# Optimization experiments

Hardware: AMD Instinct MI355X
Metric: run time of the kernel (lower is better)

## Reference

```python
import jax, jax.numpy as jnp
import numpy as np

N = 8192
D_IN, D_GAT, D_GCN = 128, 64, 64


def setup_inputs() -> dict:
    key = jax.random.key(0)
    ks = jax.random.split(key, 7)
    feat = jax.random.normal(ks[0], (N, D_IN), dtype=jnp.float32)
    r = jax.random.uniform(ks[1], (N, N), dtype=jnp.float32)
    sup = jnp.where(r < 0.01, r * 100.0, 0.0)
    xav = lambda k, shape: jax.random.normal(k, shape, dtype=jnp.float32) * jnp.sqrt(2.0 / (shape[0] + shape[1]))
    W_map = xav(ks[2], (D_IN, D_GAT))
    b_map = jnp.zeros((1,), dtype=jnp.float32)
    U = xav(ks[3], (D_GAT, 1))
    V = xav(ks[4], (D_GAT, 1))
    W_gcn = xav(ks[5], (D_GAT, D_GCN))
    return {"feat": feat, "sup": sup, "W_map": W_map, "b_map": b_map, "U": U, "V": V, "W_gcn": W_gcn}


def reference(feat, sup, W_map, b_map, U, V, W_gcn):
    n = sup.shape[0]
    sup2 = sup + jnp.eye(n, dtype=sup.dtype)  # add self-loops
    # GAT layer
    h = feat @ W_map                            # [N, D_GAT]
    s = h @ U                                   # [N, 1] score from source node i
    t = h @ V                                   # [N, 1] score from target node j
    # torch loop builds att[j, i] = tanh(s_i + t_j + b)
    att = jnp.tanh(s.T + t + b_map)             # [N, N]
    att = jnp.where(sup2 > 0, att, jnp.float32(-100.0))
    att = jax.nn.softmax(att, axis=1)
    gat_feat = jnp.tanh(att @ h)                # [N, D_GAT]
    # GCN layer (dropout is identity at inference)
    agg = sup2 @ gat_feat                       # [N, D_GAT]
    out = jax.nn.relu(agg @ W_gcn)              # [N, D_GCN]
    norm = jnp.linalg.norm(out, axis=1, keepdims=True)
    out = out / jnp.maximum(norm, jnp.float32(1e-12))  # F.normalize(p=2, dim=1)
    return out
```

## Files before the change

### kernel.cpp

```cpp
#include <hip/hip_runtime.h>


#define N_NODES 8192
#define D_IN    128
#define D_GAT   64
#define SLOTS   256

#define COMPACT4(VX, QQ)                                                      \
    {                                                                         \
        float ee[4] = {VX.x, VX.y, VX.z, VX.w};                               \
        _Pragma("unroll")                                                     \
        for (int u = 0; u < 4; ++u) {                                         \
            const int i = (QQ) * 4 + u;                                       \
            const float vv = ee[u] + ((i == j) ? 1.0f : 0.0f);      \
            const bool keep = vv > 0.f;                                       \
            const unsigned long long mask = __ballot(keep);                   \
            if (keep) {                                                       \
                const int pos = base +                                        \
                    __popcll(mask & ((1ull << lane) - 1ull));                 \
                if (pos < SLOTS) { clr[pos] = i; vvr[pos] = vv; }             \
            }                                                                 \
            base += __popcll(mask);                                           \
        }                                                                     \
    }

__global__ __launch_bounds__(256) void k1_map(
    const float* __restrict__ feat, const float* __restrict__ W_map,
    const float* __restrict__ U, const float* __restrict__ V,
    float* __restrict__ h, float* __restrict__ s, float* __restrict__ t)
{
    const int wid  = threadIdx.x >> 6;
    const int lane = threadIdx.x & 63;
    const int row = blockIdx.x * 4 + wid;
    __shared__ float f[4 * D_IN];
    if (threadIdx.x < 128)
        ((float4*)f)[threadIdx.x] =
            ((const float4*)(feat + (size_t)blockIdx.x * 4 * D_IN))[threadIdx.x];
    __syncthreads();
    const float* fr = f + wid * D_IN;
    float acc = 0.f;
#pragma unroll 8
    for (int k = 0; k < D_IN; ++k)
        acc += fr[k] * W_map[k * D_GAT + lane];
    h[row * D_GAT + lane] = acc;
    float sv = acc * U[lane];
    float tv = acc * V[lane];
#pragma unroll
    for (int off = 32; off > 0; off >>= 1) {
        sv += __shfl_xor(sv, off);
        tv += __shfl_xor(tv, off);
    }
    if (lane == 0) { s[row] = sv; t[row] = tv; }
}

__global__ __launch_bounds__(256) void k23_compact_gat(
    const float* __restrict__ sup, const float* __restrict__ h,
    const float* __restrict__ s, const float* __restrict__ t,
    const float* __restrict__ b,
    int* __restrict__ cnt, int* __restrict__ col, float* __restrict__ val,
    float* __restrict__ gat)
{
    const int wid  = threadIdx.x >> 6;
    const int lane = threadIdx.x & 63;
    const int j = blockIdx.x * 4 + wid;

    __shared__ int   cl_s[4][SLOTS];
    __shared__ float vv_s[4][SLOTS];
    __shared__ float w_s[4][SLOTS];
    int*   clr = cl_s[wid];
    float* vvr = vv_s[wid];
    float* w   = w_s[wid];

    const float4* row4 = (const float4*)(sup + (size_t)j * N_NODES);
    int base = 0;
    for (int q = lane; q < N_NODES / 4; q += 128) {
        float4 v0 = row4[q];
        float4 v1 = row4[q + 64];
        COMPACT4(v0, q);
        COMPACT4(v1, q + 64);
    }
    const int m = (base < SLOTS) ? base : SLOTS;
    __syncthreads();

    int*   colj = col + j * SLOTS;
    float* valj = val + j * SLOTS;
    const float tj = t[j] + b[0];
    float lmax = -1e30f;
    for (int p = lane; p < m; p += 64) {
        const int ci = clr[p];
        colj[p] = ci;
        valj[p] = vvr[p];
        const float e = tanhf(s[ci] + tj);
        w[p] = e;
        lmax = fmaxf(lmax, e);
    }
    if (lane == 0) cnt[j] = m;
#pragma unroll
    for (int off = 32; off > 0; off >>= 1)
        lmax = fmaxf(lmax, __shfl_xor(lmax, off));

    float lsum = 0.f;
    for (int p = lane; p < m; p += 64) {
        const float e = __expf(w[p] - lmax);
        w[p] = e;
        lsum += e;
    }
#pragma unroll
    for (int off = 32; off > 0; off >>= 1) lsum += __shfl_xor(lsum, off);
    __syncthreads();

    const int c16 = (lane & 15) * 4;
    const int pp  = lane >> 4;
    float4 a0 = make_float4(0,0,0,0), a1 = a0, a2 = a0, a3 = a0;
    for (int bse = 0; bse < m; bse += 16) {
        const int p0 = bse + pp, p1 = p0 + 4, p2 = p0 + 8, p3 = p0 + 12;
        if (p0 < m) { const float wp = w[p0];
            const float4 v = *(const float4*)(h + clr[p0] * D_GAT + c16);
            a0.x += wp*v.x; a0.y += wp*v.y; a0.z += wp*v.z; a0.w += wp*v.w; }
        if (p1 < m) { const float wp = w[p1];
            const float4 v = *(const float4*)(h + clr[p1] * D_GAT + c16);
            a1.x += wp*v.x; a1.y += wp*v.y; a1.z += wp*v.z; a1.w += wp*v.w; }
        if (p2 < m) { const float wp = w[p2];
            const float4 v = *(const float4*)(h + clr[p2] * D_GAT + c16);
            a2.x += wp*v.x; a2.y += wp*v.y; a2.z += wp*v.z; a2.w += wp*v.w; }
        if (p3 < m) { const float wp = w[p3];
            const float4 v = *(const float4*)(h + clr[p3] * D_GAT + c16);
            a3.x += wp*v.x; a3.y += wp*v.y; a3.z += wp*v.z; a3.w += wp*v.w; }
    }
    float4 acc;
    acc.x = (a0.x + a1.x) + (a2.x + a3.x);
    acc.y = (a0.y + a1.y) + (a2.y + a3.y);
    acc.z = (a0.z + a1.z) + (a2.z + a3.z);
    acc.w = (a0.w + a1.w) + (a2.w + a3.w);
#pragma unroll
    for (int off = 16; off <= 32; off <<= 1) {
        acc.x += __shfl_xor(acc.x, off); acc.y += __shfl_xor(acc.y, off);
        acc.z += __shfl_xor(acc.z, off); acc.w += __shfl_xor(acc.w, off);
    }
    if (pp == 0) {
        const float inv = 1.0f / lsum;
        float4 o;
        o.x = tanhf(acc.x * inv); o.y = tanhf(acc.y * inv);
        o.z = tanhf(acc.z * inv); o.w = tanhf(acc.w * inv);
        *(float4*)(gat + j * D_GAT + c16) = o;
    }
}

__global__ __launch_bounds__(256) void k4_gcn(
    const float* __restrict__ gat, const float* __restrict__ W_gcn,
    const int* __restrict__ cnt, const int* __restrict__ col,
    const float* __restrict__ val, float* __restrict__ out)
{
    const int wid  = threadIdx.x >> 6;
    const int lane = threadIdx.x & 63;
    const int j = blockIdx.x * 4 + wid;
    const int m = cnt[j];
    const int*   colj = col + j * SLOTS;
    const float* valj = val + j * SLOTS;
    __shared__ int   cl_s[4][SLOTS];
    __shared__ float wv_s[4][SLOTS];
    __shared__ float a_s[4][D_GAT];
    int*   cl = cl_s[wid];
    float* wv = wv_s[wid];
    float* a  = a_s[wid];
    for (int p = lane; p < m; p += 64) { cl[p] = colj[p]; wv[p] = valj[p]; }
    __syncthreads();

    const int c16 = (lane & 15) * 4;
    const int pp  = lane >> 4;
    float4 a0 = make_float4(0,0,0,0), a1 = a0, a2 = a0, a3 = a0;
    for (int base = 0; base < m; base += 16) {
        const int p0 = base + pp, p1 = p0 + 4, p2 = p0 + 8, p3 = p0 + 12;
        if (p0 < m) { const float wp = wv[p0];
            const float4 v = *(const float4*)(gat + cl[p0] * D_GAT + c16);
            a0.x += wp*v.x; a0.y += wp*v.y; a0.z += wp*v.z; a0.w += wp*v.w; }
        if (p1 < m) { const float wp = wv[p1];
            const float4 v = *(const float4*)(gat + cl[p1] * D_GAT + c16);
            a1.x += wp*v.x; a1.y += wp*v.y; a1.z += wp*v.z; a1.w += wp*v.w; }
        if (p2 < m) { const float wp = wv[p2];
            const float4 v = *(const float4*)(gat + cl[p2] * D_GAT + c16);
            a2.x += wp*v.x; a2.y += wp*v.y; a2.z += wp*v.z; a2.w += wp*v.w; }
        if (p3 < m) { const float wp = wv[p3];
            const float4 v = *(const float4*)(gat + cl[p3] * D_GAT + c16);
            a3.x += wp*v.x; a3.y += wp*v.y; a3.z += wp*v.z; a3.w += wp*v.w; }
    }
    float4 acc;
    acc.x = (a0.x + a1.x) + (a2.x + a3.x);
    acc.y = (a0.y + a1.y) + (a2.y + a3.y);
    acc.z = (a0.z + a1.z) + (a2.z + a3.z);
    acc.w = (a0.w + a1.w) + (a2.w + a3.w);
#pragma unroll
    for (int off = 16; off <= 32; off <<= 1) {
        acc.x += __shfl_xor(acc.x, off); acc.y += __shfl_xor(acc.y, off);
        acc.z += __shfl_xor(acc.z, off); acc.w += __shfl_xor(acc.w, off);
    }
    if (pp == 0) *(float4*)(a + c16) = acc;
    __syncthreads();

    float o = 0.f;
#pragma unroll 8
    for (int d = 0; d < D_GAT; ++d)
        o += a[d] * W_gcn[d * D_GAT + lane];
    o = fmaxf(o, 0.f);

    float ss = o * o;
#pragma unroll
    for (int off = 32; off > 0; off >>= 1) ss += __shfl_xor(ss, off);
    const float nrm = sqrtf(ss);
    out[j * D_GAT + lane] = o / fmaxf(nrm, 1e-12f);
}

extern "C" void kernel_launch(void* const* d_in, const int* in_sizes, int n_in,
                              void* d_out, int out_size, void* d_ws, size_t ws_size,
                              hipStream_t stream) {
    const float* feat  = (const float*)d_in[0];
    const float* sup   = (const float*)d_in[1];
    const float* W_map = (const float*)d_in[2];
    const float* b_map = (const float*)d_in[3];
    const float* U     = (const float*)d_in[4];
    const float* V     = (const float*)d_in[5];
    const float* W_gcn = (const float*)d_in[6];
    float* out = (float*)d_out;

    char* ws = (char*)d_ws;
    float* h   = (float*)(ws);
    float* gat = (float*)(ws + (2u << 20));
    float* s   = (float*)(ws + (4u << 20));
    float* t   = (float*)(ws + (4u << 20) + 32768);
    int*   cnt = (int*)  (ws + (4u << 20) + 65536);
    int*   col = (int*)  (ws + (4u << 20) + 98304);
    float* val = (float*)(ws + (12u << 20) + 98304);

    k1_map<<<N_NODES / 4, 256, 0, stream>>>(feat, W_map, U, V, h, s, t);
    k23_compact_gat<<<N_NODES / 4, 256, 0, stream>>>(
        sup, h, s, t, b_map, cnt, col, val, gat);
    k4_gcn<<<N_NODES / 4, 256, 0, stream>>>(gat, W_gcn, cnt, col, val, out);
}
```

Measured before the change: 406.2 us.

## Fuse compaction, softmax and aggregation into one streaming pass per row

The GAT kernel now computes exp(tanh(s_i+t_j)) as each nonzero is compacted and writes col/val straight to global memory. It consumes batches of 16 compacted entries into the h-aggregation while the row scan is still running, and prefetches the next float4 pair of the adjacency row. This drops the separate max and exp passes, the extra shared arrays and the block syncs, overlapping gather latency with the streaming read. It removes the max subtraction, which relies on tanh bounding the exponent, and the softmax sum is now reduced only across the 4 lane groups.

New measurement: 449.0 us. 10.5% more time.

```diff
diff --git a/kernel.cpp b/kernel.cpp
--- a/kernel.cpp
+++ b/kernel.cpp
@@ -8,20 +8,41 @@
 
 #define COMPACT4(VX, QQ)                                                      \
     {                                                                         \
-        float ee[4] = {VX.x, VX.y, VX.z, VX.w};                               \
+        float ee4[4] = {VX.x, VX.y, VX.z, VX.w};                              \
         _Pragma("unroll")                                                     \
         for (int u = 0; u < 4; ++u) {                                         \
             const int i = (QQ) * 4 + u;                                       \
-            const float vv = ee[u] + ((i == j) ? 1.0f : 0.0f);      \
+            const float vv = ee4[u] + ((i == j) ? 1.0f : 0.0f);     \
             const bool keep = vv > 0.f;                                       \
             const unsigned long long mask = __ballot(keep);                   \
             if (keep) {                                                       \
                 const int pos = base +                                        \
                     __popcll(mask & ((1ull << lane) - 1ull));                 \
-                if (pos < SLOTS) { clr[pos] = i; vvr[pos] = vv; }             \
+                if (pos < SLOTS) {                                            \
+                    clr[pos]  = i;                                            \
+                    we[pos]   = __expf(tanhf(s[i] + tj));                     \
+                    colj[pos] = i;                                            \
+                    valj[pos] = vv;                                           \
+                }                                                             \
             }                                                                 \
             base += __popcll(mask);                                           \
         }                                                                     \
+    }
+
+#define BATCH16()                                                             \
+    {                                                                         \
+        const int p0 = done + pp, p1 = p0 + 4, p2 = p0 + 8, p3 = p0 + 12;     \
+        const float e0 = we[p0], e1 = we[p1], e2 = we[p2], e3 = we[p3];       \
+        lsum += (e0 + e1) + (e2 + e3);                                        \
+        const float4 h0 = *(const float4*)(h + clr[p0] * D_GAT + c16);        \
+        const float4 h1 = *(const float4*)(h + clr[p1] * D_GAT + c16);        \
+        const float4 h2 = *(const float4*)(h + clr[p2] * D_GAT + c16);        \
+        const float4 h3 = *(const float4*)(h + clr[p3] * D_GAT + c16);        \
+        a0.x += e0*h0.x; a0.y += e0*h0.y; a0.z += e0*h0.z; a0.w += e0*h0.w;   \
+        a1.x += e1*h1.x; a1.y += e1*h1.y; a1.z += e1*h1.z; a1.w += e1*h1.w;   \
+        a2.x += e2*h2.x; a2.y += e2*h2.y; a2.z += e2*h2.z; a2.w += e2*h2.w;   \
+        a3.x += e3*h3.x; a3.y += e3*h3.y; a3.z += e3*h3.z; a3.w += e3*h3.w;   \
+        done += 16;                                                           \
     }
 
 __global__ __launch_bounds__(256) void k1_map(
@@ -65,68 +86,53 @@
     const int j = blockIdx.x * 4 + wid;
 
     __shared__ int   cl_s[4][SLOTS];
-    __shared__ float vv_s[4][SLOTS];
-    __shared__ float w_s[4][SLOTS];
+    __shared__ float we_s[4][SLOTS];
     int*   clr = cl_s[wid];
-    float* vvr = vv_s[wid];
-    float* w   = w_s[wid];
+    float* we  = we_s[wid];
+    int*   colj = col + j * SLOTS;
+    float* valj = val + j * SLOTS;
+
+    const float tj  = t[j] + b[0];
+    const int   c16 = (lane & 15) * 4;
+    const int   pp  = lane >> 4;
 
     const float4* row4 = (const float4*)(sup + (size_t)j * N_NODES);
-    int base = 0;
-    for (int q = lane; q < N_NODES / 4; q += 128) {
-        float4 v0 = row4[q];
-        float4 v1 = row4[q + 64];
+    float4 v0 = row4[lane];
+    float4 v1 = row4[lane + 64];
+    int base = 0, done = 0;
+    float lsum = 0.f;
+    float4 a0 = make_float4(0,0,0,0), a1 = a0, a2 = a0, a3 = a0;
+
+    for (int it = 0; it < 16; ++it) {
+        const int q = lane + it * 128;
+        float4 n0 = make_float4(0,0,0,0), n1 = n0;
+        if (it < 15) { n0 = row4[q + 128]; n1 = row4[q + 192]; }
         COMPACT4(v0, q);
         COMPACT4(v1, q + 64);
-    }
+        const int avail = (base < SLOTS) ? base : SLOTS;
+        while (done + 16 <= avail) BATCH16();
+        v0 = n0; v1 = n1;
+    }
+
     const int m = (base < SLOTS) ? base : SLOTS;
-    __syncthreads();
-
-    int*   colj = col + j * SLOTS;
-    float* valj = val + j * SLOTS;
-    const float tj = t[j] + b[0];
-    float lmax = -1e30f;
-    for (int p = lane; p < m; p += 64) {
-        const int ci = clr[p];
-        colj[p] = ci;
-        valj[p] = vvr[p];
-        const float e = tanhf(s[ci] + tj);
-        w[p] = e;
-        lmax = fmaxf(lmax, e);
+    while (done + 16 <= m) BATCH16();
+    {
+        const int p0 = done + pp, p1 = p0 + 4, p2 = p0 + 8, p3 = p0 + 12;
+        if (p0 < m) { const float e = we[p0]; lsum += e;
+            const float4 v = *(const float4*)(h + clr[p0] * D_GAT + c16);
+            a0.x += e*v.x; a0.y += e*v.y; a0.z += e*v.z; a0.w += e*v.w; }
+        if (p1 < m) { const float e = we[p1]; lsum += e;
+            const float4 v = *(const float4*)(h + clr[p1] * D_GAT + c16);
+            a1.x += e*v.x; a1.y += e*v.y; a1.z += e*v.z; a1.w += e*v.w; }
+        if (p2 < m) { const float e = we[p2]; lsum += e;
+            const float4 v = *(const float4*)(h + clr[p2] * D_GAT + c16);
+            a2.x += e*v.x; a2.y += e*v.y; a2.z += e*v.z; a2.w += e*v.w; }
+        if (p3 < m) { const float e = we[p3]; lsum += e;
+            const float4 v = *(const float4*)(h + clr[p3] * D_GAT + c16);
+            a3.x += e*v.x; a3.y += e*v.y; a3.z += e*v.z; a3.w += e*v.w; }
     }
     if (lane == 0) cnt[j] = m;
-#pragma unroll
-    for (int off = 32; off > 0; off >>= 1)
-        lmax = fmaxf(lmax, __shfl_xor(lmax, off));
-
-    float lsum = 0.f;
-    for (int p = lane; p < m; p += 64) {
-        const float e = __expf(w[p] - lmax);
-        w[p] = e;
-        lsum += e;
-    }
-#pragma unroll
-    for (int off = 32; off > 0; off >>= 1) lsum += __shfl_xor(lsum, off);
-    __syncthreads();
-
-    const int c16 = (lane & 15) * 4;
-    const int pp  = lane >> 4;
-    float4 a0 = make_float4(0,0,0,0), a1 = a0, a2 = a0, a3 = a0;
-    for (int bse = 0; bse < m; bse += 16) {
-        const int p0 = bse + pp, p1 = p0 + 4, p2 = p0 + 8, p3 = p0 + 12;
-        if (p0 < m) { const float wp = w[p0];
-            const float4 v = *(const float4*)(h + clr[p0] * D_GAT + c16);
-            a0.x += wp*v.x; a0.y += wp*v.y; a0.z += wp*v.z; a0.w += wp*v.w; }
-        if (p1 < m) { const float wp = w[p1];
-            const float4 v = *(const float4*)(h + clr[p1] * D_GAT + c16);
-            a1.x += wp*v.x; a1.y += wp*v.y; a1.z += wp*v.z; a1.w += wp*v.w; }
-        if (p2 < m) { const float wp = w[p2];
-            const float4 v = *(const float4*)(h + clr[p2] * D_GAT + c16);
-            a2.x += wp*v.x; a2.y += wp*v.y; a2.z += wp*v.z; a2.w += wp*v.w; }
-        if (p3 < m) { const float wp = w[p3];
-            const float4 v = *(const float4*)(h + clr[p3] * D_GAT + c16);
-            a3.x += wp*v.x; a3.y += wp*v.y; a3.z += wp*v.z; a3.w += wp*v.w; }
-    }
+
     float4 acc;
     acc.x = (a0.x + a1.x) + (a2.x + a3.x);
     acc.y = (a0.y + a1.y) + (a2.y + a3.y);
@@ -136,6 +142,7 @@
     for (int off = 16; off <= 32; off <<= 1) {
         acc.x += __shfl_xor(acc.x, off); acc.y += __shfl_xor(acc.y, off);
         acc.z += __shfl_xor(acc.z, off); acc.w += __shfl_xor(acc.w, off);
+        lsum  += __shfl_xor(lsum, off);
     }
     if (pp == 0) {
         const float inv = 1.0f / lsum;
```
